# Kernel optimization log

Hardware: AMD Instinct MI355X
Metric: run time of the kernel (lower is better)

Reference implementation:

```python
import jax, jax.numpy as jnp
import numpy as np

IN_FEATURES = 1024
OUT_FEATURES = 1024
BATCH = 32
SEQ = 1024
EPS = 1e-8


def setup_inputs() -> dict:
    key = jax.random.key(0)
    k1, k2, k3 = jax.random.split(key, 3)
    Efou = jax.random.normal(k1, (BATCH, SEQ, IN_FEATURES), dtype=jnp.float32)
    y = jax.random.normal(k2, (BATCH, IN_FEATURES), dtype=jnp.float32)
    weight = jax.random.normal(k3, (IN_FEATURES, OUT_FEATURES), dtype=jnp.float32)
    return {"Efou": Efou, "y": y, "weight": weight}


def reference(Efou, y, weight):
    # scale = 1/sqrt(in_features)
    scale = 1.0 / np.sqrt(np.float32(weight.shape[0]))
    ys = y * scale  # (b, i) == per-sample column scaling of weight
    # Demodulation norm: sum_i (scale*W[i,o]*y[b,i])^2 = (ys^2) @ (W^2)
    d = jax.lax.rsqrt(jnp.einsum('bi,io->bo', ys * ys, weight * weight) + EPS)  # (b, o)
    # Efou @ (scale*W*y*d) == ((Efou*ys) @ W) * d  -- same math, avoids (b,i,o) weight
    out = jnp.einsum('bsi,io->bso', Efou * ys[:, None, :], weight) * d[:, None, :]
    return out
```

## Files before the change

### kernel.cpp

```cpp
#include <hip/hip_runtime.h>

#define AS1 __attribute__((address_space(1)))
#define AS3 __attribute__((address_space(3)))

typedef __bf16 bf16x8 __attribute__((ext_vector_type(8)));
typedef float f32x4 __attribute__((ext_vector_type(4)));
typedef unsigned short ushort8 __attribute__((ext_vector_type(8)));

__device__ __forceinline__ unsigned short f2bf(float f) {
  union { float f; unsigned u; } v; v.f = f;
  unsigned u = v.u;
  unsigned r = (u + 0x7fffu + ((u >> 16) & 1u)) >> 16;
  return (unsigned short)r;
}

__global__ __launch_bounds__(256) void prep_kernel(const float* __restrict__ y,
                                                   const float* __restrict__ W,
                                                   float* __restrict__ partial,
                                                   unsigned short* __restrict__ WT) {
  __shared__ float ysq[32][32];
  const int o = blockIdx.x * 256 + threadIdx.x;
  const int i0 = blockIdx.y * 32;
  for (int e = threadIdx.x; e < 1024; e += 256) {
    int il = e >> 5, b = e & 31;
    float t = y[b * 1024 + i0 + il] * 0.03125f;
    ysq[il][b] = t * t;
  }
  __syncthreads();

  f32x4 acc[8] = {};
  ushort8 wb[4];
#pragma unroll
  for (int il = 0; il < 32; ++il) {
    float w = W[(size_t)(i0 + il) * 1024 + o];
    wb[il >> 3][il & 7] = f2bf(w);
    float w2 = w * w;
#pragma unroll
    for (int b4 = 0; b4 < 8; ++b4) {
      f32x4 q = *(const f32x4*)&ysq[il][b4 * 4];
#pragma unroll
      for (int k = 0; k < 4; ++k) acc[b4][k] = fmaf(q[k], w2, acc[b4][k]);
    }
  }
  unsigned short* wt = WT + (size_t)o * 1024 + i0;
#pragma unroll
  for (int q = 0; q < 4; ++q) *(ushort8*)(wt + q * 8) = wb[q];
  float* p = partial + (size_t)blockIdx.y * 32768 + o;
#pragma unroll
  for (int b4 = 0; b4 < 8; ++b4)
#pragma unroll
    for (int k = 0; k < 4; ++k) p[(b4 * 4 + k) * 1024] = acc[b4][k];
}

#define NT 16
#define LDS_TILE 65536

#define BAR __builtin_amdgcn_s_barrier()
#define LGKM0 asm volatile("s_waitcnt lgkmcnt(0)" ::: "memory")
#define VM(n) asm volatile("s_waitcnt vmcnt(" #n ")" ::: "memory")
#define SCHB __builtin_amdgcn_sched_barrier(0)
#define PRIO(x) __builtin_amdgcn_s_setprio(x)

#define STG_B(r, t, dst)                                                     \
  __builtin_amdgcn_global_load_lds(                                          \
      (const AS1 void*)(Ws + (size_t)(r) * 64 * 2048 + (t) * 128),           \
      (AS3 void*)((dst) + 32768 + (r) * 8192 + sldso), 16, 0, 0)

#define A_ISSUE(t)                                                           \
  {                                                                          \
    const float* asrc = Efou + (size_t)(m0 + argp * 4) * 1024 + (t) * 64 + k8; \
    _Pragma("unroll") for (int rr = 0; rr < 4; ++rr) {                       \
      pa[rr][0] = *(const f32x4*)(asrc + rr * 1024);                         \
      pa[rr][1] = *(const f32x4*)(asrc + rr * 1024 + 4);                     \
    }                                                                        \
    yv[0] = *(const f32x4*)(ysS + (t) * 64 + k8);                            \
    yv[1] = *(const f32x4*)(ysS + (t) * 64 + k8 + 4);                        \
  }

#define ACVT_WR(dst)                                                         \
  {                                                                          \
    _Pragma("unroll") for (int rr = 0; rr < 4; ++rr) {                       \
      const int row = argp * 4 + rr;                                         \
      ushort8 ov;                                                            \
      _Pragma("unroll") for (int q = 0; q < 4; ++q) {                        \
        ov[q] = f2bf(pa[rr][0][q] * yv[0][q]);                               \
        ov[q + 4] = f2bf(pa[rr][1][q] * yv[1][q]);                           \
      }                                                                      \
      *(ushort8*)((dst) + row * 128 + ((kslot * 16) ^ ((row & 7) << 4))) = ov; \
    }                                                                        \
  }

#define RD_A(mh, mi, kk)                                                     \
  (*(const bf16x8*)(Ab + (wr * 128 + ((mh) * 4 + (mi)) * 16 + l15) * 128 +   \
                    ((((kk) * 64 + lhi * 16)) ^ swz_rd)))
#define RD_B(nh, ni, kk)                                                     \
  (*(const bf16x8*)(Bb + (wc * 64 + ((nh) * 2 + (ni)) * 16 + l15) * 128 +    \
                    ((((kk) * 64 + lhi * 16)) ^ swz_rd)))

#define LD_A(mh)                                                             \
  { _Pragma("unroll") for (int mi = 0; mi < 4; ++mi)                         \
      _Pragma("unroll") for (int kk = 0; kk < 2; ++kk)                       \
        a[mi][kk] = RD_A(mh, mi, kk); }
#define LD_B(nh)                                                             \
  { _Pragma("unroll") for (int ni = 0; ni < 2; ++ni)                         \
      _Pragma("unroll") for (int kk = 0; kk < 2; ++kk)                       \
        bfr[ni][kk] = RD_B(nh, ni, kk); }

#define MM(mh, nh)                                                           \
  do {                                                                       \
    _Pragma("unroll") for (int mi = 0; mi < 4; ++mi)                         \
      _Pragma("unroll") for (int ni = 0; ni < 2; ++ni)                       \
        _Pragma("unroll") for (int kk = 0; kk < 2; ++kk)                     \
          acc[(mh) * 4 + mi][(nh) * 2 + ni] =                                \
              __builtin_amdgcn_mfma_f32_16x16x32_bf16(                       \
                  a[mi][kk], bfr[ni][kk], acc[(mh) * 4 + mi][(nh) * 2 + ni], \
                  0, 0, 0);                                                  \
  } while (0)

__global__ __launch_bounds__(512, 2) void gemmf3_kernel(
    const float* __restrict__ Efou, const float* __restrict__ y,
    const unsigned short* __restrict__ WT, const float* __restrict__ dpart,
    float* __restrict__ out) {
  extern __shared__ char lds[];
  float* ysS = (float*)(lds + 2 * LDS_TILE);
  float* dtab = (float*)(lds + 2 * LDS_TILE + 4096);

  const int tid = threadIdx.x;
  const int bid = blockIdx.x;
  const int wg = (bid & 7) * 64 + (bid >> 3);
  const int bm = wg >> 2, bn = wg & 3;
  const int m0 = bm * 256, n0 = bn * 256;
  const int b = m0 >> 10;

  const int w = tid >> 6, l = tid & 63;
  const int wr = w >> 2, wc = w & 3;
  const int l15 = l & 15, lhi = l >> 4;
  const int swz_rd = (l15 & 7) << 4;

  const int kslot = tid & 7;
  const int k8 = kslot * 8;
  const int argp = tid >> 3;

  const int srow = tid >> 3;
  const int scb = ((tid & 7) << 4) ^ ((srow & 7) << 4);
  const char* Ws = (const char*)WT + (size_t)(n0 + srow) * 2048 + scb;
  const int sldso = tid * 16;

  f32x4 acc[8][4] = {};
  bf16x8 a[4][2], bfr[2][2];
  f32x4 pa[4][2], yv[2];

  if (tid < 256) {
    const float* dp = dpart + b * 1024 + n0 + tid;
    float s = 0.f;
#pragma unroll 8
    for (int is = 0; is < 32; ++is) s += dp[(size_t)is * 32768];
    dtab[tid] = rsqrtf(s + 1e-8f);
  }
  {
    float2 yy = *(const float2*)(y + b * 1024 + tid * 2);
    ysS[2 * tid] = yy.x * 0.03125f;
    ysS[2 * tid + 1] = yy.y * 0.03125f;
  }
  __syncthreads();
  {
    char* d0 = lds;
    STG_B(0, 0, d0); STG_B(1, 0, d0); STG_B(2, 0, d0); STG_B(3, 0, d0);
    A_ISSUE(0);
    A_WRITE_PROLOGUE:
    ACVT_WR(d0);
  }
  VM(0); LGKM0; BAR;

  for (int t = 0; t < NT - 1; ++t) {
    const char* Ab = lds + (t & 1) * LDS_TILE;
    const char* Bb = Ab + 32768;
    char* dN = lds + ((t & 1) ^ 1) * LDS_TILE;
    const int t1 = t + 1;
    LD_A(0); LD_B(0);
    A_ISSUE(t1);
    STG_B(0, t1, dN); STG_B(1, t1, dN);
    BAR; LGKM0; SCHB; PRIO(1); MM(0, 0); PRIO(0); SCHB; BAR;
    LD_B(1);
    STG_B(2, t1, dN); STG_B(3, t1, dN);
    BAR; LGKM0; SCHB; PRIO(1); MM(0, 1); PRIO(0); SCHB; BAR;
    LD_A(1); LD_B(0);
    ACVT_WR(dN);
    BAR; LGKM0; SCHB; PRIO(1); MM(1, 0); PRIO(0); SCHB; BAR;
    LD_B(1);
    BAR; LGKM0; SCHB; PRIO(1); MM(1, 1); PRIO(0); SCHB;
    VM(0);
    LGKM0;
    BAR;
  }

  {
    const char* Ab = lds + ((NT - 1) & 1) * LDS_TILE;
    const char* Bb = Ab + 32768;
    LD_A(0); LD_B(0);
    BAR; LGKM0; SCHB; PRIO(1); MM(0, 0); PRIO(0); SCHB; BAR;
    LD_B(1);
    BAR; LGKM0; SCHB; PRIO(1); MM(0, 1); PRIO(0); SCHB; BAR;
    LD_A(1); LD_B(0);
    BAR; LGKM0; SCHB; PRIO(1); MM(1, 0); PRIO(0); SCHB; BAR;
    LD_B(1);
    BAR; LGKM0; SCHB; PRIO(1); MM(1, 1); PRIO(0); SCHB;
  }

  const int lc0 = wc * 64 + l15;
  float dv[4];
#pragma unroll
  for (int nf = 0; nf < 4; ++nf) dv[nf] = dtab[lc0 + nf * 16];
#pragma unroll
  for (int mf = 0; mf < 8; ++mf) {
#pragma unroll
    for (int j = 0; j < 4; ++j) {
      const int row = m0 + wr * 128 + mf * 16 + lhi * 4 + j;
      float* orow = out + (size_t)row * 1024 + n0 + lc0;
#pragma unroll
      for (int nf = 0; nf < 4; ++nf) orow[nf * 16] = acc[mf][nf][j] * dv[nf];
    }
  }
}

extern "C" void kernel_launch(void* const* d_in, const int* in_sizes, int n_in,
                              void* d_out, int out_size, void* d_ws, size_t ws_size,
                              hipStream_t stream) {
  const float* Efou = (const float*)d_in[0];
  const float* y    = (const float*)d_in[1];
  const float* W    = (const float*)d_in[2];
  float* out = (float*)d_out;

  unsigned short* WT = (unsigned short*)d_ws;
  float* dpart       = (float*)(WT + (size_t)1024 * 1024);

  hipFuncSetAttribute((const void*)gemmf3_kernel,
                      hipFuncAttributeMaxDynamicSharedMemorySize, 136192);

  prep_kernel<<<dim3(4, 32), 256, 0, stream>>>(y, W, dpart, WT);
  gemmf3_kernel<<<512, 512, 136192, stream>>>(Efou, y, WT, dpart, out);
}
```

Before: 134.3 us.

## Move demodulation reduction to separate kernel and fold A-tile write into MFMA phase

Pulls the 32-way partial-sum reduction and rsqrt out of every GEMM block into a small dedicated kernel that writes the demodulation vector once, so each GEMM block reads only its needed values in the epilogue instead of redoing the strided reduction in its prologue. It also moves the converted A-tile LDS write inside the third MFMA phase, after the barrier, so the writes can interleave with the matrix ops. The cost is an extra kernel launch and a global read in the epilogue, plus slightly less LDS per block.

```diff
diff --git a/kernel.cpp b/kernel.cpp
--- a/kernel.cpp
+++ b/kernel.cpp
@@ -52,6 +52,15 @@
     for (int k = 0; k < 4; ++k) p[(b4 * 4 + k) * 1024] = acc[b4][k];
 }
 
+__global__ __launch_bounds__(256) void dcalc_b_kernel(const float* __restrict__ partial,
+                                                      float* __restrict__ dmod) {
+  const int bo = blockIdx.x * 256 + threadIdx.x;
+  float acc = 0.f;
+#pragma unroll 8
+  for (int is = 0; is < 32; ++is) acc += partial[(size_t)is * 32768 + bo];
+  dmod[bo] = rsqrtf(acc + 1e-8f);
+}
+
 #define NT 16
 #define LDS_TILE 65536
 
@@ -117,13 +126,12 @@
                   0, 0, 0);                                                  \
   } while (0)
 
-__global__ __launch_bounds__(512, 2) void gemmf3_kernel(
+__global__ __launch_bounds__(512, 2) void gemmf4_kernel(
     const float* __restrict__ Efou, const float* __restrict__ y,
-    const unsigned short* __restrict__ WT, const float* __restrict__ dpart,
+    const unsigned short* __restrict__ WT, const float* __restrict__ dmod,
     float* __restrict__ out) {
   extern __shared__ char lds[];
   float* ysS = (float*)(lds + 2 * LDS_TILE);
-  float* dtab = (float*)(lds + 2 * LDS_TILE + 4096);
 
   const int tid = threadIdx.x;
   const int bid = blockIdx.x;
@@ -150,13 +158,6 @@
   bf16x8 a[4][2], bfr[2][2];
   f32x4 pa[4][2], yv[2];
 
-  if (tid < 256) {
-    const float* dp = dpart + b * 1024 + n0 + tid;
-    float s = 0.f;
-#pragma unroll 8
-    for (int is = 0; is < 32; ++is) s += dp[(size_t)is * 32768];
-    dtab[tid] = rsqrtf(s + 1e-8f);
-  }
   {
     float2 yy = *(const float2*)(y + b * 1024 + tid * 2);
     ysS[2 * tid] = yy.x * 0.03125f;
@@ -167,7 +168,6 @@
     char* d0 = lds;
     STG_B(0, 0, d0); STG_B(1, 0, d0); STG_B(2, 0, d0); STG_B(3, 0, d0);
     A_ISSUE(0);
-    A_WRITE_PROLOGUE:
     ACVT_WR(d0);
   }
   VM(0); LGKM0; BAR;
@@ -185,8 +185,10 @@
     STG_B(2, t1, dN); STG_B(3, t1, dN);
     BAR; LGKM0; SCHB; PRIO(1); MM(0, 1); PRIO(0); SCHB; BAR;
     LD_A(1); LD_B(0);
+    BAR; LGKM0; SCHB; PRIO(1);
     ACVT_WR(dN);
-    BAR; LGKM0; SCHB; PRIO(1); MM(1, 0); PRIO(0); SCHB; BAR;
+    MM(1, 0);
+    PRIO(0); SCHB; BAR;
     LD_B(1);
     BAR; LGKM0; SCHB; PRIO(1); MM(1, 1); PRIO(0); SCHB;
     VM(0);
@@ -207,16 +209,16 @@
     BAR; LGKM0; SCHB; PRIO(1); MM(1, 1); PRIO(0); SCHB;
   }
 
-  const int lc0 = wc * 64 + l15;
+  const int col0 = n0 + wc * 64 + l15;
   float dv[4];
 #pragma unroll
-  for (int nf = 0; nf < 4; ++nf) dv[nf] = dtab[lc0 + nf * 16];
+  for (int nf = 0; nf < 4; ++nf) dv[nf] = dmod[b * 1024 + col0 + nf * 16];
 #pragma unroll
   for (int mf = 0; mf < 8; ++mf) {
 #pragma unroll
     for (int j = 0; j < 4; ++j) {
       const int row = m0 + wr * 128 + mf * 16 + lhi * 4 + j;
-      float* orow = out + (size_t)row * 1024 + n0 + lc0;
+      float* orow = out + (size_t)row * 1024 + col0;
 #pragma unroll
       for (int nf = 0; nf < 4; ++nf) orow[nf * 16] = acc[mf][nf][j] * dv[nf];
     }
@@ -233,10 +235,12 @@
 
   unsigned short* WT = (unsigned short*)d_ws;
   float* dpart       = (float*)(WT + (size_t)1024 * 1024);
-
-  hipFuncSetAttribute((const void*)gemmf3_kernel,
-                      hipFuncAttributeMaxDynamicSharedMemorySize, 136192);
+  float* dmod        = dpart + (size_t)32 * 32768;
+
+  hipFuncSetAttribute((const void*)gemmf4_kernel,
+                      hipFuncAttributeMaxDynamicSharedMemorySize, 135168);
 
   prep_kernel<<<dim3(4, 32), 256, 0, stream>>>(y, W, dpart, WT);
-  gemmf3_kernel<<<512, 512, 136192, stream>>>(Efou, y, WT, dpart, out);
-}
+  dcalc_b_kernel<<<128, 256, 0, stream>>>(dpart, dmod);
+  gemmf4_kernel<<<512, 512, 135168, stream>>>(Efou, y, WT, dmod, out);
+}
```

New measurement: 127.9 us. 1.05x faster.
